# Optimization experiments

Hardware: AMD Instinct MI355X
Metric: run time of the kernel (lower is better)

Reference implementation:

```python
import jax, jax.numpy as jnp
import numpy as np

N_S = 50000   # support points
N_Q = 50000   # query points
H = 32        # neighbors per query
K = 15        # kernel points
C_IN = 64
C_OUT = 64
G = 8         # group norm groups
RADIUS = 1.0
SIGMA = 0.6
EPS = 1e-5
NEG_SLOPE = 0.1


def setup_inputs() -> dict:
    key = jax.random.key(0)
    ks = jax.random.split(key, 8)
    s_feats = jax.random.normal(ks[0], (N_S, C_IN), jnp.float32)
    q_points = jax.random.uniform(ks[1], (N_Q, 3), jnp.float32)
    s_points = jax.random.uniform(ks[2], (N_S, 3), jnp.float32)
    # index N_S is the shadow (padding) neighbor
    neighbor_indices = jax.random.randint(ks[3], (N_Q, H), 0, N_S + 1)
    # kernel point dispositions: fixed points inside a ball of RADIUS
    d = jax.random.normal(ks[4], (K, 3), jnp.float32)
    d = d / jnp.linalg.norm(d, axis=1, keepdims=True)
    r = jax.random.uniform(ks[5], (K, 1), jnp.float32) ** (1.0 / 3.0)
    kernel_points = d * r * RADIUS                      # (K,3)
    weights = jax.random.normal(ks[6], (K, C_IN, C_OUT), jnp.float32) * (1.0 / np.sqrt(K * C_IN))
    bias = jax.random.normal(ks[7], (C_OUT,), jnp.float32) * 0.01
    gamma = jnp.ones((C_OUT,), jnp.float32)
    beta = jnp.zeros((C_OUT,), jnp.float32)
    return dict(s_feats=s_feats, q_points=q_points, s_points=s_points,
                neighbor_indices=neighbor_indices, kernel_points=kernel_points,
                weights=weights, bias=bias, gamma=gamma, beta=beta)


def kpconv(s_feats, q_points, s_points, neighbor_indices, kernel_points, weights, bias):
    # pad support set with shadow point (1e10) and zero features
    pad_pts = jnp.concatenate([s_points, jnp.full((1, 3), 1e10, s_points.dtype)], axis=0)
    pad_feats = jnp.concatenate([s_feats, jnp.zeros((1, s_feats.shape[1]), s_feats.dtype)], axis=0)
    nbr_pts = pad_pts[neighbor_indices] - q_points[:, None, :]              # (M,H,3)
    diff = nbr_pts[:, :, None, :] - kernel_points[None, None, :, :]         # (M,H,K,3)
    sq_d = jnp.sum(diff * diff, axis=-1)                                    # (M,H,K)
    # linear correlation influence, clamped at 0
    w = jnp.maximum(1.0 - jnp.sqrt(sq_d) / SIGMA, 0.0)                      # (M,H,K)
    nbr_feats = pad_feats[neighbor_indices]                                 # (M,H,Cin)
    weighted = jnp.einsum('mhk,mhc->mkc', w, nbr_feats)                     # (M,K,Cin)
    out = jnp.einsum('mkc,kcd->md', weighted, weights)                      # (M,Cout)
    # normalize by number of valid neighbors (feature-sum > 0 test, as in KPConv)
    nbr_num = jnp.sum(jnp.sum(nbr_feats, axis=-1) > 0, axis=-1)             # (M,)
    nbr_num = jnp.maximum(nbr_num, 1).astype(out.dtype)
    return out / nbr_num[:, None] + bias


def group_norm(x, gamma, beta):
    # matches GroupNorm wrapper: (M,C) -> (1,C,M) -> nn.GroupNorm -> (M,C)
    M, C = x.shape
    xg = x.T.reshape(G, C // G, M)                                          # (G,Cg,M)
    mean = xg.mean(axis=(1, 2), keepdims=True)
    var = xg.var(axis=(1, 2), keepdims=True)
    xn = ((xg - mean) / jnp.sqrt(var + EPS)).reshape(C, M).T                # (M,C)
    return xn * gamma + beta


def reference(s_feats, q_points, s_points, neighbor_indices, kernel_points, weights, bias, gamma, beta):
    x = kpconv(s_feats, q_points, s_points, neighbor_indices, kernel_points, weights, bias)
    x = group_norm(x, gamma, beta)
    x = jnp.where(x >= 0, x, NEG_SLOPE * x)                                 # LeakyReLU(0.1)
    return x[:, None, :]                                                    # unsqueeze(1): (M,1,Cout)
```

## Files before the change

kernel.cpp:

```cpp
#include <hip/hip_runtime.h>
#include <hip/hip_bf16.h>
#include <math.h>

#define NSUP 50000
#define NQ   50000
#define NH   32
#define NK   15
#define NG   8
#define INV_SIGMA (1.0f/0.6f)
#define GN_EPS 1e-5f
#define NEG  0.1f

#define QB   16
#define NBLK (NQ/QB)

#define OFF_ROWSUM 0
#define OFF_FB     50048
#define OFF_WB     (OFF_FB + 1600000)
#define OFF_PS     (OFF_WB + 30720)
#define OFF_PQ     (OFF_PS + NBLK*8)
#define OFF_STAT   (OFF_PQ + NBLK*8)

typedef __attribute__((ext_vector_type(8))) short bf16x8;
typedef __attribute__((ext_vector_type(4))) float f32x4;
typedef __attribute__((ext_vector_type(4))) unsigned int u32x4;

__device__ __forceinline__ short f2bf(float x) {
    __hip_bfloat16 h = __float2bfloat16(x);
    return *reinterpret_cast<short*>(&h);
}

__global__ __launch_bounds__(256) void k_prep(const float* __restrict__ sf,
                                              float* __restrict__ rowsum,
                                              unsigned short* __restrict__ fb) {
    int row  = (blockIdx.x * 256 + threadIdx.x) >> 6;
    int lane = threadIdx.x & 63;
    if (row >= NSUP) return;
    float v = sf[(size_t)row * 64 + lane];
    fb[(size_t)row * 64 + lane] = (unsigned short)f2bf(v);
    float s = v;
    #pragma unroll
    for (int o = 32; o; o >>= 1) s += __shfl_down(s, o);
    if (lane == 0) rowsum[row] = s;
}

__global__ __launch_bounds__(256) void k_wpack(const float* __restrict__ wts,
                                               unsigned short* __restrict__ wb) {
    int idx = blockIdx.x * 256 + threadIdx.x;
    if (idx >= 30 * 4 * 64 * 8) return;
    int j  = idx & 7;
    int l  = (idx >> 3) & 63;
    int n  = (idx >> 9) & 3;
    int ks = idx >> 11;
    int r  = ks * 32 + ((l >> 4) << 3) + j;
    int d  = n * 16 + (l & 15);
    wb[idx] = (unsigned short)f2bf(wts[(size_t)r * 64 + d]);
}

__global__ __launch_bounds__(256, 5) void k_conv(
    const unsigned short* __restrict__ fb, const float* __restrict__ qpts,
    const float* __restrict__ spts,  const int*   __restrict__ nidx,
    const float* __restrict__ kpts,  const unsigned short* __restrict__ wb,
    const float* __restrict__ bias,  const float* __restrict__ rowsum,
    float* __restrict__ conv_out, float* __restrict__ part_s, float* __restrict__ part_q)
{
    __shared__ __align__(16) short wl16[16 * 968];
    __shared__ __align__(16) float kp4[16][4];
    __shared__ float rcl[16];

    const int tid  = threadIdx.x;
    const int wv   = tid >> 6;
    const int lane = tid & 63;
    const int g    = lane >> 4;
    const int c16  = lane & 15;

    if (tid < 16) {
        if (tid < NK) {
            kp4[tid][0] = kpts[tid*3+0];
            kp4[tid][1] = kpts[tid*3+1];
            kp4[tid][2] = kpts[tid*3+2];
        } else {
            kp4[tid][0] = 1e8f; kp4[tid][1] = 1e8f; kp4[tid][2] = 1e8f;
        }
        kp4[tid][3] = 0.f;
    }
    __syncthreads();

    const float kx = kp4[c16][0], ky = kp4[c16][1], kz = kp4[c16][2];

    const int qbase = blockIdx.x * QB;
    char* WV = (char*)wl16 + wv * 6144;
    f32x4* XY = (f32x4*)WV;
    char*  FP = WV + 1024;

    f32x4 pacc[4][4];
    #pragma unroll
    for (int a = 0; a < 4; a++)
        #pragma unroll
        for (int b = 0; b < 4; b++) pacc[a][b] = (f32x4){0.f,0.f,0.f,0.f};

    const int h    = lane & 31;
    const int half = lane >> 5;

    #pragma unroll
    for (int pp = 0; pp < 2; pp++) {
        {
            const int qq = pp*2 + half;
            const int m  = qbase + wv*4 + qq;
            const float qx = qpts[m*3+0], qy = qpts[m*3+1], qz = qpts[m*3+2];
            const int  id  = nidx[(size_t)m * NH + h];
            const bool val = (id < NSUP);
            const int  ii  = val ? id : 0;
            const float dx = spts[ii*3+0]-qx, dy = spts[ii*3+1]-qy, dz = spts[ii*3+2]-qz;
            const float rs = rowsum[ii];
            unsigned long long bal = __ballot(val && rs > 0.f);
            int cA = __popcll(bal & 0xffffffffull); if (cA < 1) cA = 1;
            int cB = __popcll(bal >> 32);           if (cB < 1) cB = 1;
            if (lane == 0)  rcl[wv*4 + pp*2]     = 1.0f / (float)cA;
            if (lane == 32) rcl[wv*4 + pp*2 + 1] = 1.0f / (float)cB;
            f32x4 st; st.x = val ? dx : 1e10f; st.y = dy; st.z = dz; st.w = 0.f;
            XY[half*32 + h] = st;
        }

        #pragma unroll
        for (int e = 0; e < 2; e++) {
            const int q2 = pp*2 + e;
            const int m2 = qbase + wv*4 + q2;

            union { unsigned short u[8]; bf16x8 v; } ua;
            #pragma unroll
            for (int j = 0; j < 8; j++) {
                f32x4 p = XY[e*32 + g*8 + j];
                float ex = p.x - kx, ey = p.y - ky, ez = p.z - kz;
                float sq = fmaf(ex, ex, fmaf(ey, ey, ez * ez));
                float w  = fmaxf(1.0f - sqrtf(sq) * INV_SIGMA, 0.f);
                ua.u[j]  = (unsigned short)f2bf(w);
            }

            #pragma unroll
            for (int i = 0; i < 4; i++) {
                const int r = i*8 + (lane >> 3);
                const int s = lane & 7;
                int id2 = nidx[(size_t)m2 * NH + r];
                id2 = (id2 < NSUP) ? id2 : 0;
                u32x4 v = *(const u32x4*)((const char*)fb + (size_t)id2*128 + s*16);
                *(u32x4*)(FP + r*144 + ((s ^ (i & 3)) << 4)) = v;
            }

            #pragma unroll
            for (int ct = 0; ct < 4; ct++) {
                const char* vb = FP + (g*8)*144
                               + (((((ct << 1) | (c16 >> 3)) ^ g) & 7) << 4)
                               + ((c16 & 7) << 1);
                union { unsigned short u[8]; bf16x8 v; } ub;
                #pragma unroll
                for (int j = 0; j < 8; j++)
                    ub.u[j] = *(const unsigned short*)(vb + j*144);
                pacc[q2][ct] = __builtin_amdgcn_mfma_f32_16x16x32_bf16(ua.v, ub.v, pacc[q2][ct], 0, 0, 0);
            }
        }
    }

    __syncthreads();

    #pragma unroll
    for (int qq = 0; qq < 4; qq++) {
        #pragma unroll
        for (int ct = 0; ct < 4; ct++) {
            #pragma unroll
            for (int i = 0; i < 4; i++) {
                const int kk = g*4 + i;
                if (kk < NK)
                    wl16[(wv*4 + qq)*968 + kk*64 + ct*16 + c16] = f2bf(pacc[qq][ct][i]);
            }
        }
    }
    __syncthreads();

    f32x4 facc = (f32x4){0.f,0.f,0.f,0.f};
    const short* ap = wl16 + (lane & 15)*968 + (lane >> 4)*8;
    const unsigned short* bp = wb + ((size_t)(wv * 64 + lane)) * 8;
    #pragma unroll 6
    for (int ks = 0; ks < 30; ks++) {
        bf16x8 a = *(const bf16x8*)(ap + ks*32);
        bf16x8 b = *(const bf16x8*)(bp + (size_t)ks*2048);
        facc = __builtin_amdgcn_mfma_f32_16x16x32_bf16(a, b, facc, 0, 0, 0);
    }

    const int   d  = wv*16 + (lane & 15);
    const float bs = bias[d];
    float gl = 0.f, gq = 0.f;
    #pragma unroll
    for (int i = 0; i < 4; i++) {
        const int row = (lane >> 4)*4 + i;
        const float y = facc[i] * rcl[row] + bs;
        conv_out[(size_t)(qbase + row)*64 + d] = y;
        gl += y;
        gq = fmaf(y, y, gq);
    }
    #pragma unroll
    for (int msk = 1; msk <= 4; msk <<= 1) { gl += __shfl_xor(gl, msk); gq += __shfl_xor(gq, msk); }
    gl += __shfl_xor(gl, 16); gq += __shfl_xor(gq, 16);
    gl += __shfl_xor(gl, 32); gq += __shfl_xor(gq, 32);
    if ((lane & 55) == 0) {
        const int grp = wv*2 + (lane >> 3);
        part_s[(size_t)blockIdx.x * 8 + grp] = gl;
        part_q[(size_t)blockIdx.x * 8 + grp] = gq;
    }
}

__global__ __launch_bounds__(1024) void k_reduce(const float* __restrict__ part_s,
                                                 const float* __restrict__ part_q,
                                                 float* __restrict__ stat) {
    __shared__ double ds[128][8], dq[128][8];
    const int t = threadIdx.x;
    const int g = t & 7, chunk = t >> 3;
    const int per = (NBLK + 127) / 128;
    double s = 0.0, q = 0.0;
    int lo = chunk * per, hi = lo + per; if (hi > NBLK) hi = NBLK;
    for (int i = lo; i < hi; i++) {
        s += (double)part_s[(size_t)i * 8 + g];
        q += (double)part_q[(size_t)i * 8 + g];
    }
    ds[chunk][g] = s; dq[chunk][g] = q;
    __syncthreads();
    if (t < 8) {
        double S = 0.0, Q = 0.0;
        for (int cix = 0; cix < 128; cix++) { S += ds[cix][t]; Q += dq[cix][t]; }
        const double cnt = (double)(64 / NG) * (double)NQ;
        double mean = S / cnt;
        double var  = Q / cnt - mean * mean;
        stat[t]     = (float)mean;
        stat[8 + t] = (float)(1.0 / sqrt(var + (double)GN_EPS));
    }
}

__global__ __launch_bounds__(256) void k_apply(float* __restrict__ out,
                                               const float* __restrict__ stat,
                                               const float* __restrict__ gamma,
                                               const float* __restrict__ beta) {
    const int n4 = NQ * 64 / 4;
    for (int idx = blockIdx.x * 256 + threadIdx.x; idx < n4; idx += gridDim.x * 256) {
        float4 v = ((const float4*)out)[idx];
        const int c4 = idx & 15;
        const int g  = c4 >> 1;
        const float mean = stat[g], istd = stat[8 + g];
        const float4 ga = ((const float4*)gamma)[c4];
        const float4 be = ((const float4*)beta)[c4];
        float4 r;
        r.x = (v.x - mean) * istd * ga.x + be.x; r.x = r.x >= 0.f ? r.x : NEG * r.x;
        r.y = (v.y - mean) * istd * ga.y + be.y; r.y = r.y >= 0.f ? r.y : NEG * r.y;
        r.z = (v.z - mean) * istd * ga.z + be.z; r.z = r.z >= 0.f ? r.z : NEG * r.z;
        r.w = (v.w - mean) * istd * ga.w + be.w; r.w = r.w >= 0.f ? r.w : NEG * r.w;
        ((float4*)out)[idx] = r;
    }
}

extern "C" void kernel_launch(void* const* d_in, const int* in_sizes, int n_in,
                              void* d_out, int out_size, void* d_ws, size_t ws_size,
                              hipStream_t stream) {
    const float* sfeats = (const float*)d_in[0];
    const float* qpts   = (const float*)d_in[1];
    const float* spts   = (const float*)d_in[2];
    const int*   nidx   = (const int*)  d_in[3];
    const float* kpts   = (const float*)d_in[4];
    const float* wts    = (const float*)d_in[5];
    const float* bias   = (const float*)d_in[6];
    const float* gamma  = (const float*)d_in[7];
    const float* beta   = (const float*)d_in[8];

    float* ws = (float*)d_ws;
    float*          rowsum = ws + OFF_ROWSUM;
    unsigned short* fb     = (unsigned short*)(ws + OFF_FB);
    unsigned short* wb     = (unsigned short*)(ws + OFF_WB);
    float*          ps     = ws + OFF_PS;
    float*          pq     = ws + OFF_PQ;
    float*          stat   = ws + OFF_STAT;
    float*          out    = (float*)d_out;

    k_prep <<<dim3((NSUP + 3) / 4), dim3(256), 0, stream>>>(sfeats, rowsum, fb);
    k_wpack<<<dim3(240),            dim3(256), 0, stream>>>(wts, wb);
    k_conv <<<dim3(NBLK),           dim3(256), 0, stream>>>(fb, qpts, spts, nidx, kpts,
                                                            wb, bias, rowsum, out, ps, pq);
    k_reduce<<<dim3(1),   dim3(1024), 0, stream>>>(ps, pq, stat);
    k_apply <<<dim3(1024), dim3(256), 0, stream>>>(out, stat, gamma, beta);
}
```

Baseline: 82.00 us.

## Prefetch neighbor features, shuffle offsets in registers, swizzle LDS, merge prep kernels

Merges the weight-packing kernel into the feature-prep kernel to drop one launch. In the conv kernel, neighbor offsets stay in registers and are broadcast with shuffles instead of being staged through LDS. The next query's neighbor feature gathers are software-pipelined, issued before the current MFMAs. The bf16 intermediate tile written to LDS gets an XOR swizzle to reduce bank conflicts on the second GEMM's A loads. Costs are more registers for the prefetch buffers and extra shuffle instructions in the weight computation.

```diff
diff --git a/kernel.cpp b/kernel.cpp
--- a/kernel.cpp
+++ b/kernel.cpp
@@ -32,29 +32,30 @@
 
 __global__ __launch_bounds__(256) void k_prep(const float* __restrict__ sf,
                                               float* __restrict__ rowsum,
-                                              unsigned short* __restrict__ fb) {
-    int row  = (blockIdx.x * 256 + threadIdx.x) >> 6;
-    int lane = threadIdx.x & 63;
-    if (row >= NSUP) return;
-    float v = sf[(size_t)row * 64 + lane];
-    fb[(size_t)row * 64 + lane] = (unsigned short)f2bf(v);
-    float s = v;
-    #pragma unroll
-    for (int o = 32; o; o >>= 1) s += __shfl_down(s, o);
-    if (lane == 0) rowsum[row] = s;
-}
-
-__global__ __launch_bounds__(256) void k_wpack(const float* __restrict__ wts,
-                                               unsigned short* __restrict__ wb) {
-    int idx = blockIdx.x * 256 + threadIdx.x;
-    if (idx >= 30 * 4 * 64 * 8) return;
-    int j  = idx & 7;
-    int l  = (idx >> 3) & 63;
-    int n  = (idx >> 9) & 3;
-    int ks = idx >> 11;
-    int r  = ks * 32 + ((l >> 4) << 3) + j;
-    int d  = n * 16 + (l & 15);
-    wb[idx] = (unsigned short)f2bf(wts[(size_t)r * 64 + d]);
+                                              unsigned short* __restrict__ fb,
+                                              const float* __restrict__ wts,
+                                              unsigned short* __restrict__ wb) {
+    if (blockIdx.x < 12500) {
+        int row  = (blockIdx.x * 256 + threadIdx.x) >> 6;
+        int lane = threadIdx.x & 63;
+        if (row >= NSUP) return;
+        float v = sf[(size_t)row * 64 + lane];
+        fb[(size_t)row * 64 + lane] = (unsigned short)f2bf(v);
+        float s = v;
+        #pragma unroll
+        for (int o = 32; o; o >>= 1) s += __shfl_down(s, o);
+        if (lane == 0) rowsum[row] = s;
+    } else {
+        int idx = (blockIdx.x - 12500) * 256 + threadIdx.x;
+        if (idx >= 30 * 4 * 64 * 8) return;
+        int j  = idx & 7;
+        int l  = (idx >> 3) & 63;
+        int n  = (idx >> 9) & 3;
+        int ks = idx >> 11;
+        int r  = ks * 32 + ((l >> 4) << 3) + j;
+        int d  = n * 16 + (l & 15);
+        wb[idx] = (unsigned short)f2bf(wts[(size_t)r * 64 + d]);
+    }
 }
 
 __global__ __launch_bounds__(256, 5) void k_conv(
@@ -89,9 +90,7 @@
     const float kx = kp4[c16][0], ky = kp4[c16][1], kz = kp4[c16][2];
 
     const int qbase = blockIdx.x * QB;
-    char* WV = (char*)wl16 + wv * 6144;
-    f32x4* XY = (f32x4*)WV;
-    char*  FP = WV + 1024;
+    char* FP = (char*)wl16 + wv * 6144;
 
     f32x4 pacc[4][4];
     #pragma unroll
@@ -102,62 +101,85 @@
     const int h    = lane & 31;
     const int half = lane >> 5;
 
+    float dxr[2], dyr[2], dzr[2];
     #pragma unroll
     for (int pp = 0; pp < 2; pp++) {
-        {
-            const int qq = pp*2 + half;
-            const int m  = qbase + wv*4 + qq;
-            const float qx = qpts[m*3+0], qy = qpts[m*3+1], qz = qpts[m*3+2];
-            const int  id  = nidx[(size_t)m * NH + h];
-            const bool val = (id < NSUP);
-            const int  ii  = val ? id : 0;
-            const float dx = spts[ii*3+0]-qx, dy = spts[ii*3+1]-qy, dz = spts[ii*3+2]-qz;
-            const float rs = rowsum[ii];
-            unsigned long long bal = __ballot(val && rs > 0.f);
-            int cA = __popcll(bal & 0xffffffffull); if (cA < 1) cA = 1;
-            int cB = __popcll(bal >> 32);           if (cB < 1) cB = 1;
-            if (lane == 0)  rcl[wv*4 + pp*2]     = 1.0f / (float)cA;
-            if (lane == 32) rcl[wv*4 + pp*2 + 1] = 1.0f / (float)cB;
-            f32x4 st; st.x = val ? dx : 1e10f; st.y = dy; st.z = dz; st.w = 0.f;
-            XY[half*32 + h] = st;
-        }
-
-        #pragma unroll
-        for (int e = 0; e < 2; e++) {
-            const int q2 = pp*2 + e;
-            const int m2 = qbase + wv*4 + q2;
-
-            union { unsigned short u[8]; bf16x8 v; } ua;
+        const int qq = pp*2 + half;
+        const int m  = qbase + wv*4 + qq;
+        const float qx = qpts[m*3+0], qy = qpts[m*3+1], qz = qpts[m*3+2];
+        const int  id  = nidx[(size_t)m * NH + h];
+        const bool val = (id < NSUP);
+        const int  ii  = val ? id : 0;
+        const float dx = spts[ii*3+0]-qx, dy = spts[ii*3+1]-qy, dz = spts[ii*3+2]-qz;
+        const float rs = rowsum[ii];
+        unsigned long long bal = __ballot(val && rs > 0.f);
+        int cA = __popcll(bal & 0xffffffffull); if (cA < 1) cA = 1;
+        int cB = __popcll(bal >> 32);           if (cB < 1) cB = 1;
+        if (lane == 0)  rcl[wv*4 + pp*2]     = 1.0f / (float)cA;
+        if (lane == 32) rcl[wv*4 + pp*2 + 1] = 1.0f / (float)cB;
+        dxr[pp] = val ? dx : 1e10f; dyr[pp] = dy; dzr[pp] = dz;
+    }
+
+    const int gr = lane >> 3;
+    const int gs = lane & 7;
+    int   idp[4];
+    u32x4 vp[4];
+    {
+        const int m0 = qbase + wv*4;
+        #pragma unroll
+        for (int i = 0; i < 4; i++) idp[i] = nidx[(size_t)m0*NH + i*8 + gr];
+        #pragma unroll
+        for (int i = 0; i < 4; i++) {
+            const int id2 = (idp[i] < NSUP) ? idp[i] : 0;
+            vp[i] = *(const u32x4*)((const char*)fb + (size_t)id2*128 + gs*16);
+        }
+    }
+
+    #pragma unroll
+    for (int q = 0; q < 4; q++) {
+        const int pp = q >> 1, e = q & 1;
+
+        #pragma unroll
+        for (int i = 0; i < 4; i++)
+            *(u32x4*)(FP + (i*8 + gr)*144 + ((gs ^ i) << 4)) = vp[i];
+
+        if (q < 3) {
+            const int mn = qbase + wv*4 + q + 1;
             #pragma unroll
-            for (int j = 0; j < 8; j++) {
-                f32x4 p = XY[e*32 + g*8 + j];
-                float ex = p.x - kx, ey = p.y - ky, ez = p.z - kz;
-                float sq = fmaf(ex, ex, fmaf(ey, ey, ez * ez));
-                float w  = fmaxf(1.0f - sqrtf(sq) * INV_SIGMA, 0.f);
-                ua.u[j]  = (unsigned short)f2bf(w);
-            }
-
+            for (int i = 0; i < 4; i++) idp[i] = nidx[(size_t)mn*NH + i*8 + gr];
+        }
+
+        union { unsigned short u[8]; bf16x8 v; } ua;
+        #pragma unroll
+        for (int j = 0; j < 8; j++) {
+            const int sl = e*32 + g*8 + j;
+            const float px = __shfl(dxr[pp], sl);
+            const float py = __shfl(dyr[pp], sl);
+            const float pz = __shfl(dzr[pp], sl);
+            const float ex = px - kx, ey = py - ky, ez = pz - kz;
+            const float sq = fmaf(ex, ex, fmaf(ey, ey, ez * ez));
+            const float w  = fmaxf(1.0f - sqrtf(sq) * INV_SIGMA, 0.f);
+            ua.u[j] = (unsigned short)f2bf(w);
+        }
+
+        if (q < 3) {
             #pragma unroll
             for (int i = 0; i < 4; i++) {
-                const int r = i*8 + (lane >> 3);
-                const int s = lane & 7;
-                int id2 = nidx[(size_t)m2 * NH + r];
-                id2 = (id2 < NSUP) ? id2 : 0;
-                u32x4 v = *(const u32x4*)((const char*)fb + (size_t)id2*128 + s*16);
-                *(u32x4*)(FP + r*144 + ((s ^ (i & 3)) << 4)) = v;
+                const int id2 = (idp[i] < NSUP) ? idp[i] : 0;
+                vp[i] = *(const u32x4*)((const char*)fb + (size_t)id2*128 + gs*16);
             }
-
+        }
+
+        #pragma unroll
+        for (int ct = 0; ct < 4; ct++) {
+            const char* vb = FP + (g*8)*144
+                           + (((((ct << 1) | (c16 >> 3)) ^ g) & 7) << 4)
+                           + ((c16 & 7) << 1);
+            union { unsigned short u[8]; bf16x8 v; } ub;
             #pragma unroll
-            for (int ct = 0; ct < 4; ct++) {
-                const char* vb = FP + (g*8)*144
-                               + (((((ct << 1) | (c16 >> 3)) ^ g) & 7) << 4)
-                               + ((c16 & 7) << 1);
-                union { unsigned short u[8]; bf16x8 v; } ub;
-                #pragma unroll
-                for (int j = 0; j < 8; j++)
-                    ub.u[j] = *(const unsigned short*)(vb + j*144);
-                pacc[q2][ct] = __builtin_amdgcn_mfma_f32_16x16x32_bf16(ua.v, ub.v, pacc[q2][ct], 0, 0, 0);
-            }
+            for (int j = 0; j < 8; j++)
+                ub.u[j] = *(const unsigned short*)(vb + j*144);
+            pacc[q][ct] = __builtin_amdgcn_mfma_f32_16x16x32_bf16(ua.v, ub.v, pacc[q][ct], 0, 0, 0);
         }
     }
 
@@ -170,29 +192,35 @@
             #pragma unroll
             for (int i = 0; i < 4; i++) {
                 const int kk = g*4 + i;
-                if (kk < NK)
-                    wl16[(wv*4 + qq)*968 + kk*64 + ct*16 + c16] = f2bf(pacc[qq][ct][i]);
+                if (kk < NK) {
+                    const int ch = kk*8 + ct*2 + (c16 >> 3);
+                    const int sc = ch ^ ((ch >> 5) & 3);
+                    wl16[(wv*4 + qq)*968 + sc*8 + (c16 & 7)] = f2bf(pacc[qq][ct][i]);
+                }
             }
         }
     }
     __syncthreads();
 
     f32x4 facc = (f32x4){0.f,0.f,0.f,0.f};
-    const short* ap = wl16 + (lane & 15)*968 + (lane >> 4)*8;
+    const int z = lane >> 4;
+    const short* arow = wl16 + c16*968;
     const unsigned short* bp = wb + ((size_t)(wv * 64 + lane)) * 8;
     #pragma unroll 6
     for (int ks = 0; ks < 30; ks++) {
-        bf16x8 a = *(const bf16x8*)(ap + ks*32);
+        const int L  = ks*4 + z;
+        const int sL = L ^ ((L >> 5) & 3);
+        bf16x8 a = *(const bf16x8*)(arow + sL*8);
         bf16x8 b = *(const bf16x8*)(bp + (size_t)ks*2048);
         facc = __builtin_amdgcn_mfma_f32_16x16x32_bf16(a, b, facc, 0, 0, 0);
     }
 
-    const int   d  = wv*16 + (lane & 15);
+    const int   d  = wv*16 + c16;
     const float bs = bias[d];
     float gl = 0.f, gq = 0.f;
     #pragma unroll
     for (int i = 0; i < 4; i++) {
-        const int row = (lane >> 4)*4 + i;
+        const int row = z*4 + i;
         const float y = facc[i] * rcl[row] + bs;
         conv_out[(size_t)(qbase + row)*64 + d] = y;
         gl += y;
@@ -278,10 +306,9 @@
     float*          stat   = ws + OFF_STAT;
     float*          out    = (float*)d_out;
 
-    k_prep <<<dim3((NSUP + 3) / 4), dim3(256), 0, stream>>>(sfeats, rowsum, fb);
-    k_wpack<<<dim3(240),            dim3(256), 0, stream>>>(wts, wb);
-    k_conv <<<dim3(NBLK),           dim3(256), 0, stream>>>(fb, qpts, spts, nidx, kpts,
-                                                            wb, bias, rowsum, out, ps, pq);
-    k_reduce<<<dim3(1),   dim3(1024), 0, stream>>>(ps, pq, stat);
+    k_prep <<<dim3(12740), dim3(256), 0, stream>>>(sfeats, rowsum, fb, wts, wb);
+    k_conv <<<dim3(NBLK),  dim3(256), 0, stream>>>(fb, qpts, spts, nidx, kpts,
+                                                   wb, bias, rowsum, out, ps, pq);
+    k_reduce<<<dim3(1),    dim3(1024), 0, stream>>>(ps, pq, stat);
     k_apply <<<dim3(1024), dim3(256), 0, stream>>>(out, stat, gamma, beta);
 }
```

After: 81.47 us. About the same (-0.6%).
